# Kernel tuning notes

Measured on AMD Instinct MI355X. Metric: run time of the kernel, lower is better.

## Reference

```python
import jax, jax.numpy as jnp
import numpy as np

C = 64          # channels
K = 15          # sum(shell_sizes)=1+14
H = 32          # neighbors per query
N = 50000       # support points (== query points M)
RADIUS = 1.0
SIGMA = 0.7
INF = 1e6
BN_EPS = 1e-5


def _init_kernel_points(key):
    # stand-in for load_kernels: 1 center point + 14 points on a sphere shell
    pts = jax.random.normal(key, (K - 1, 3), dtype=jnp.float32)
    pts = pts / jnp.linalg.norm(pts, axis=1, keepdims=True) * RADIUS
    return jnp.concatenate([jnp.zeros((1, 3), jnp.float32), pts], axis=0)


def setup_inputs() -> dict:
    key = jax.random.key(0)
    ks = jax.random.split(key, 10)
    q_pts = jax.random.normal(ks[0], (N, 3), dtype=jnp.float32)
    s_pts = jax.random.normal(ks[1], (N, 3), dtype=jnp.float32)
    s_feats = jax.random.normal(ks[2], (N, C), dtype=jnp.float32)
    neighb_inds = jax.random.randint(ks[3], (N, H), 0, N)
    kernel_points = _init_kernel_points(ks[4])
    # alpha_mlp: Linear(C->C, no bias) -> BatchNorm -> LeakyReLU(0.1) -> Linear(C->K*C)
    lim1 = 1.0 / np.sqrt(C)
    W1 = jax.random.uniform(ks[5], (C, C), jnp.float32, -lim1, lim1)
    gamma = jnp.ones((C,), jnp.float32)
    beta = jnp.zeros((C,), jnp.float32)
    W2 = jax.random.uniform(ks[6], (C, K * C), jnp.float32, -lim1, lim1)
    b2 = jax.random.uniform(ks[7], (K * C,), jnp.float32, -lim1, lim1)
    return {"q_pts": q_pts, "s_pts": s_pts, "s_feats": s_feats,
            "neighb_inds": neighb_inds, "kernel_points": kernel_points,
            "W1": W1, "gamma": gamma, "beta": beta, "W2": W2, "b2": b2}


def reference(q_pts, s_pts, s_feats, neighb_inds, kernel_points, W1, gamma, beta, W2, b2):
    M = q_pts.shape[0]
    # alpha_mlp on pooled (= center) features: (M, C) -> (M, K*C)
    h = s_feats @ W1
    mu = jnp.mean(h, axis=0)
    var = jnp.var(h, axis=0)
    h = (h - mu) / jnp.sqrt(var + BN_EPS) * gamma + beta
    h = jax.nn.leaky_relu(h, 0.1)
    conv_weights = (h @ W2 + b2).reshape(M, K, C)

    # gather neighbor features with a zero padding row (index N -> zeros)
    padded_feats = jnp.concatenate([s_feats, jnp.zeros((1, C), s_feats.dtype)], axis=0)
    neighbor_feats = padded_feats[neighb_inds]                 # (M, H, C)

    # relative neighbor positions with inf padding point
    s_pts_pad = jnp.concatenate([s_pts, jnp.full((1, 3), INF, s_pts.dtype)], axis=0)
    neighbors = s_pts_pad[neighb_inds] - q_pts[:, None, :]     # (M, H, 3)

    # kernel-point influence: nearest kernel point + linear influence
    diff = neighbors[:, :, None, :] - kernel_points            # (M, H, K, 3)
    sq_d = jnp.sum(diff * diff, axis=-1)                       # (M, H, K)
    nn_sq = jnp.min(sq_d, axis=-1)                             # (M, H)
    nn_idx = jnp.argmin(sq_d, axis=-1)                         # (M, H)
    infl = jnp.clip(1.0 - jnp.sqrt(nn_sq) / SIGMA, 0.0)        # (M, H)

    # per-neighbor channel weights from the MLP output, gathered by 1nn kernel point
    nw = jnp.take_along_axis(conv_weights, nn_idx[:, :, None], axis=1)  # (M, H, C)
    nw = nw * infl[:, :, None]

    # weighted aggregation (merge=mul, aggr=sum over neighbors)
    return jnp.sum(neighbor_feats * nw, axis=1)                # (M, C)
```

## Files before the change

kernel.cpp:

```cpp
#include <hip/hip_runtime.h>
#include <math.h>

#define N_PTS 50000
#define CCH   64
#define KP    15
#define NH    32
#define SIGMA 0.7f
#define BN_EPS 1e-5f
#define LEAKY 0.1f
#define QB    16
#define STATS_BLOCKS 1024
#define SP4_BLOCKS 196
#define CW_KSTRIDE_B 2176

typedef short bf16x8 __attribute__((ext_vector_type(8)));
typedef float floatx4 __attribute__((ext_vector_type(4)));

__device__ __forceinline__ unsigned short f2b(float f) {
    union { float f; unsigned u; } v; v.f = f;
    return (unsigned short)((v.u + 0x7FFFu + ((v.u >> 16) & 1u)) >> 16);
}
__device__ __forceinline__ float b2f(unsigned short b) {
    union { unsigned u; float f; } v; v.u = ((unsigned)b) << 16;
    return v.f;
}
__device__ __forceinline__ float blo(unsigned u) {
    union { unsigned u; float f; } v; v.u = u << 16;
    return v.f;
}
__device__ __forceinline__ float bhi(unsigned u) {
    union { unsigned u; float f; } v; v.u = u & 0xFFFF0000u;
    return v.f;
}
__device__ __forceinline__ unsigned cvtpk(float lo, float hi) {
    unsigned r;
    asm("v_cvt_pk_bf16_f32 %0, %1, %2" : "=v"(r) : "v"(lo), "v"(hi));
    return r;
}

__global__ __launch_bounds__(256) void k_prep(const float* __restrict__ sf,
                                              const float* __restrict__ W1,
                                              const float* __restrict__ W2,
                                              const float* __restrict__ s_pts,
                                              const float* __restrict__ kpts,
                                              float* __restrict__ bn,
                                              unsigned short* __restrict__ hst,
                                              unsigned short* __restrict__ w2b,
                                              unsigned short* __restrict__ sfb,
                                              float* __restrict__ sp4,
                                              float* __restrict__ kpc4) {
    int t = threadIdx.x;
    if (blockIdx.x >= STATS_BLOCKS + 30 + SP4_BLOCKS) {
        if (t < KP) {
            float x = kpts[t * 3 + 0], y = kpts[t * 3 + 1], z = kpts[t * 3 + 2];
            float4 v; v.x = x; v.y = y; v.z = z; v.w = 0.5f * (x * x + y * y + z * z);
            *(float4*)(kpc4 + t * 4) = v;
        }
        return;
    }
    if (blockIdx.x >= STATS_BLOCKS + 30) {
        int g = (blockIdx.x - STATS_BLOCKS - 30) * 256 + t;
        if (g < N_PTS) {
            float4 v;
            v.x = s_pts[g * 3 + 0]; v.y = s_pts[g * 3 + 1];
            v.z = s_pts[g * 3 + 2]; v.w = 0.f;
            *(float4*)(sp4 + g * 4) = v;
        }
        return;
    }
    if (blockIdx.x >= STATS_BLOCKS) {
        int g = (blockIdx.x - STATS_BLOCKS) * 256 + t;
        int lane = g & 63, s = (g >> 6) & 1, tt = g >> 7;
        int col = lane & 15, quad = lane >> 4;
        int base = (s * 32 + quad * 8) * 960 + tt * 16 + col;
        ushort4 lo, hi;
        lo.x = f2b(W2[base + 0 * 960]); lo.y = f2b(W2[base + 1 * 960]);
        lo.z = f2b(W2[base + 2 * 960]); lo.w = f2b(W2[base + 3 * 960]);
        hi.x = f2b(W2[base + 4 * 960]); hi.y = f2b(W2[base + 5 * 960]);
        hi.z = f2b(W2[base + 6 * 960]); hi.w = f2b(W2[base + 7 * 960]);
        *(ushort4*)(w2b + g * 8)     = lo;
        *(ushort4*)(w2b + g * 8 + 4) = hi;
        return;
    }
    int c = t & 63, ml = t >> 6;
    float w1c[64];
    #pragma unroll
    for (int i = 0; i < 64; ++i) w1c[i] = W1[i * 64 + c];
    __shared__ float rows[16][64];
    float acc_s = 0.f, acc_q = 0.f;
    for (int tile = blockIdx.x; tile < N_PTS / 16; tile += STATS_BLOCKS) {
        int m0 = tile * 16;
        __syncthreads();
        float4 v = *(const float4*)(sf + m0 * 64 + t * 4);
        ((float4*)rows)[t] = v;
        ushort4 s4;
        s4.x = f2b(v.x); s4.y = f2b(v.y); s4.z = f2b(v.z); s4.w = f2b(v.w);
        *(ushort4*)(sfb + m0 * 64 + t * 4) = s4;
        __syncthreads();
        #pragma unroll
        for (int rr = 0; rr < 4; ++rr) {
            int r = ml + rr * 4;
            float h = 0.f;
            #pragma unroll
            for (int i4 = 0; i4 < 16; ++i4) {
                float4 rv = *(const float4*)&rows[r][i4 * 4];
                h += rv.x * w1c[i4 * 4] + rv.y * w1c[i4 * 4 + 1]
                   + rv.z * w1c[i4 * 4 + 2] + rv.w * w1c[i4 * 4 + 3];
            }
            acc_s += h;
            acc_q += h * h;
            hst[(m0 + r) * 64 + c] = f2b(h);
        }
    }
    __shared__ float red[2][256];
    red[0][t] = acc_s; red[1][t] = acc_q;
    __syncthreads();
    if (t < 64) {
        float s = red[0][t] + red[0][64 + t] + red[0][128 + t] + red[0][192 + t];
        float q = red[1][t] + red[1][64 + t] + red[1][128 + t] + red[1][192 + t];
        atomicAdd(&bn[t], s);
        atomicAdd(&bn[64 + t], q);
    }
}

__global__ __launch_bounds__(256, 4) void k_main(
    const float* __restrict__ q_pts, const float* __restrict__ sp4,
    const unsigned short* __restrict__ sfb, const int* __restrict__ nb,
    const float* __restrict__ kpc4, const float* __restrict__ gamma,
    const float* __restrict__ beta, const float* __restrict__ bn,
    const float* __restrict__ b2, const unsigned short* __restrict__ w2b,
    const unsigned short* __restrict__ hst, float* __restrict__ out) {

    __shared__ __align__(16) unsigned cwP[KP * 32 * 17];
    __shared__ float abS[128];
    __shared__ int      nCnt[QB];
    __shared__ unsigned nPack[QB][NH];
    __shared__ float    nInf[QB][NH];

    int t = threadIdx.x;
    int lane = t & 63, wv = t >> 6;
    int m0 = blockIdx.x * QB;

    int q0 = t >> 5, hh = t & 31;
    int q1 = q0 + 8;
    int idx0 = nb[(m0 + q0) * NH + hh];
    int idx1 = nb[(m0 + q1) * NH + hh];

    if (t < 64) {
        float mu  = bn[t] * (1.0f / N_PTS);
        float var = bn[64 + t] * (1.0f / N_PTS) - mu * mu;
        float a   = gamma[t] * rsqrtf(var + BN_EPS);
        abS[t]      = a;
        abS[64 + t] = beta[t] - mu * a;
    }
    ((unsigned*)nPack)[t]       = 0u;
    ((unsigned*)nPack)[t + 256] = 0u;
    ((float*)nInf)[t]           = 0.f;
    ((float*)nInf)[t + 256]     = 0.f;

    int row = lane & 15, half = lane >> 4;
    bf16x8 r0, r1;
    {
        const unsigned short* hrow = hst + (m0 + row) * 64 + half * 8;
        r0 = *(const bf16x8*)(hrow);
        r1 = *(const bf16x8*)(hrow + 32);
    }

    float4 sp0 = *(const float4*)(sp4 + idx0 * 4);
    float4 sp1 = *(const float4*)(sp4 + idx1 * 4);
    float qx0 = q_pts[(m0 + q0) * 3 + 0], qy0 = q_pts[(m0 + q0) * 3 + 1],
          qz0 = q_pts[(m0 + q0) * 3 + 2];
    float qx1 = q_pts[(m0 + q1) * 3 + 0], qy1 = q_pts[(m0 + q1) * 3 + 1],
          qz1 = q_pts[(m0 + q1) * 3 + 2];

    float4 kq[KP];
    #pragma unroll
    for (int i = 0; i < KP; ++i) kq[i] = *(const float4*)(kpc4 + i * 4);

    __syncthreads();

    unsigned pf0 = 0, pf1 = 0, pf2 = 0, pf3 = 0;
    {
        float px = sp0.x - qx0, py = sp0.y - qy0, pz = sp0.z - qz0;
        float pn = px * px + py * py + pz * pz;
        float best = 1e30f; int bi = 0;
        #pragma unroll
        for (int k = 0; k < KP; ++k) {
            float val = kq[k].w - (px * kq[k].x + py * kq[k].y + pz * kq[k].z);
            if (val < best) { best = val; bi = k; }
        }
        float d2 = fmaxf(fmaf(2.f, best, pn), 0.f);
        float infl = 1.f - sqrtf(d2) * (1.0f / SIGMA);
        bool keep = infl > 0.f;
        unsigned long long bal = __ballot(keep);
        unsigned mym = (unsigned)(bal >> (lane & 32));
        int pos = __popc(mym & ((1u << (lane & 31)) - 1u));
        if (keep) {
            nPack[q0][pos] = (unsigned)idx0 | ((unsigned)(bi * CW_KSTRIDE_B) << 16);
            nInf[q0][pos]  = infl;
            const unsigned* rowp = (const unsigned*)(sfb + idx0 * 64);
            pf0 = rowp[0]; pf1 = rowp[16];
        }
        if ((lane & 31) == 0) nCnt[q0] = __popc(mym);
    }
    {
        float px = sp1.x - qx1, py = sp1.y - qy1, pz = sp1.z - qz1;
        float pn = px * px + py * py + pz * pz;
        float best = 1e30f; int bi = 0;
        #pragma unroll
        for (int k = 0; k < KP; ++k) {
            float val = kq[k].w - (px * kq[k].x + py * kq[k].y + pz * kq[k].z);
            if (val < best) { best = val; bi = k; }
        }
        float d2 = fmaxf(fmaf(2.f, best, pn), 0.f);
        float infl = 1.f - sqrtf(d2) * (1.0f / SIGMA);
        bool keep = infl > 0.f;
        unsigned long long bal = __ballot(keep);
        unsigned mym = (unsigned)(bal >> (lane & 32));
        int pos = __popc(mym & ((1u << (lane & 31)) - 1u));
        if (keep) {
            nPack[q1][pos] = (unsigned)idx1 | ((unsigned)(bi * CW_KSTRIDE_B) << 16);
            nInf[q1][pos]  = infl;
            const unsigned* rowp = (const unsigned*)(sfb + idx1 * 64);
            pf2 = rowp[0]; pf3 = rowp[16];
        }
        if ((lane & 31) == 0) nCnt[q1] = __popc(mym);
    }

    bf16x8 a0, a1;
    {
        unsigned* A0 = (unsigned*)&a0;
        unsigned* A1 = (unsigned*)&a1;
        #pragma unroll
        for (int jw = 0; jw < 4; ++jw) {
            int c0 = half * 8 + jw * 2;
            float g00 = abS[c0]     * b2f((unsigned short)r0[jw * 2])     + abS[64 + c0];
            float g01 = abS[c0 + 1] * b2f((unsigned short)r0[jw * 2 + 1]) + abS[64 + c0 + 1];
            g00 = fmaxf(g00, LEAKY * g00);
            g01 = fmaxf(g01, LEAKY * g01);
            A0[jw] = cvtpk(g00, g01);
            int c1 = 32 + c0;
            float g10 = abS[c1]     * b2f((unsigned short)r1[jw * 2])     + abS[64 + c1];
            float g11 = abS[c1 + 1] * b2f((unsigned short)r1[jw * 2 + 1]) + abS[64 + c1 + 1];
            g10 = fmaxf(g10, LEAKY * g10);
            g11 = fmaxf(g11, LEAKY * g11);
            A1[jw] = cvtpk(g10, g11);
        }
    }

    {
        int colq = lane & 15, quad = lane >> 4;
        bf16x8 Lf[3], Ls[3], Mf[3], Ms[3];
        #pragma unroll
        for (int i = 0; i < 3; ++i) {
            int tt = wv * 15 + i;
            Lf[i] = *(const bf16x8*)(w2b + ((tt * 2 + 0) * 64 + lane) * 8);
            Ls[i] = *(const bf16x8*)(w2b + ((tt * 2 + 1) * 64 + lane) * 8);
        }
        #pragma unroll
        for (int g = 0; g < 5; ++g) {
            if (g < 4) {
                #pragma unroll
                for (int i = 0; i < 3; ++i) {
                    int tt = wv * 15 + (g + 1) * 3 + i;
                    Mf[i] = *(const bf16x8*)(w2b + ((tt * 2 + 0) * 64 + lane) * 8);
                    Ms[i] = *(const bf16x8*)(w2b + ((tt * 2 + 1) * 64 + lane) * 8);
                }
            }
            #pragma unroll
            for (int i = 0; i < 3; ++i) {
                int tt = wv * 15 + g * 3 + i;
                floatx4 acc = {0.f, 0.f, 0.f, 0.f};
                acc = __builtin_amdgcn_mfma_f32_16x16x32_bf16(Lf[i], a0, acc, 0, 0, 0);
                acc = __builtin_amdgcn_mfma_f32_16x16x32_bf16(Ls[i], a1, acc, 0, 0, 0);
                int n0 = tt * 16 + quad * 4;
                float4 bb = *(const float4*)&b2[n0];
                int k  = n0 >> 6;
                int c2 = (n0 & 63) >> 1;
                unsigned w0 = cvtpk(acc[0] + bb.x, acc[1] + bb.y);
                unsigned w1 = cvtpk(acc[2] + bb.z, acc[3] + bb.w);
                unsigned* dst = cwP + (k * 544 + c2 * 17 + colq);
                dst[0]  = w0;
                dst[17] = w1;
            }
            if (g < 4) {
                #pragma unroll
                for (int i = 0; i < 3; ++i) { Lf[i] = Mf[i]; Ls[i] = Ms[i]; }
            }
        }
    }
    asm volatile("" :: "v"(pf0), "v"(pf1), "v"(pf2), "v"(pf3));
    __syncthreads();

    {
        int r = lane >> 5, c2 = lane & 31;
        const unsigned short* sfbC = sfb + c2 * 2;
        const unsigned char* cwB = (const unsigned char*)cwP;
        #pragma unroll
        for (int pp = 0; pp < 2; ++pp) {
            int qa = wv * 4 + pp * 2;
            int q  = qa + r;
            const unsigned* packRow = &nPack[q][0];
            const float*    infRow  = &nInf[q][0];
            const unsigned char* cwLane = cwB + (c2 * 17 + q) * 4;
            int nA = nCnt[qa], nB = nCnt[qa + 1];
            int na = nA > nB ? nA : nB;
            float acc0 = 0.f, acc1 = 0.f;
            for (int jj = 0; jj < na; jj += 4) {
                uint4  pk = *(const uint4*)&packRow[jj];
                float4 in = *(const float4*)&infRow[jj];
                unsigned f0 = *(const unsigned*)(sfbC + (pk.x & 0xFFFFu) * 64);
                unsigned f1 = *(const unsigned*)(sfbC + (pk.y & 0xFFFFu) * 64);
                unsigned f2 = *(const unsigned*)(sfbC + (pk.z & 0xFFFFu) * 64);
                unsigned f3 = *(const unsigned*)(sfbC + (pk.w & 0xFFFFu) * 64);
                unsigned w0 = *(const unsigned*)(cwLane + (pk.x >> 16));
                unsigned w1 = *(const unsigned*)(cwLane + (pk.y >> 16));
                unsigned w2 = *(const unsigned*)(cwLane + (pk.z >> 16));
                unsigned w3 = *(const unsigned*)(cwLane + (pk.w >> 16));
                acc0 = fmaf(in.x * blo(f0), blo(w0), acc0);
                acc1 = fmaf(in.x * bhi(f0), bhi(w0), acc1);
                acc0 = fmaf(in.y * blo(f1), blo(w1), acc0);
                acc1 = fmaf(in.y * bhi(f1), bhi(w1), acc1);
                acc0 = fmaf(in.z * blo(f2), blo(w2), acc0);
                acc1 = fmaf(in.z * bhi(f2), bhi(w2), acc1);
                acc0 = fmaf(in.w * blo(f3), blo(w3), acc0);
                acc1 = fmaf(in.w * bhi(f3), bhi(w3), acc1);
            }
            float2 o; o.x = acc0; o.y = acc1;
            *(float2*)&out[(m0 + q) * 64 + c2 * 2] = o;
        }
    }
}

extern "C" void kernel_launch(void* const* d_in, const int* in_sizes, int n_in,
                              void* d_out, int out_size, void* d_ws, size_t ws_size,
                              hipStream_t stream) {
    const float* q_pts   = (const float*)d_in[0];
    const float* s_pts   = (const float*)d_in[1];
    const float* s_feats = (const float*)d_in[2];
    const int*   nb      = (const int*)d_in[3];
    const float* kpts    = (const float*)d_in[4];
    const float* W1      = (const float*)d_in[5];
    const float* gamma   = (const float*)d_in[6];
    const float* beta    = (const float*)d_in[7];
    const float* W2      = (const float*)d_in[8];
    const float* b2      = (const float*)d_in[9];
    float* out = (float*)d_out;

    float* ws = (float*)d_ws;
    float* bn = ws;
    unsigned short* w2b = (unsigned short*)(ws + 128);
    unsigned short* hst = w2b + 61440;
    unsigned short* sfb = hst + N_PTS * CCH;
    float* sp4 = (float*)(sfb + N_PTS * CCH);
    float* kpc4 = sp4 + N_PTS * 4;

    hipMemsetAsync(bn, 0, 128 * sizeof(float), stream);
    k_prep<<<STATS_BLOCKS + 30 + SP4_BLOCKS + 1, 256, 0, stream>>>(
        s_feats, W1, W2, s_pts, kpts, bn, hst, w2b, sfb, sp4, kpc4);
    k_main<<<N_PTS / QB, 256, 0, stream>>>(q_pts, sp4, sfb, nb, kpc4,
                                           gamma, beta, bn, b2, w2b, hst, out);
}
```

Baseline: 152.8 us.

## Process 32 queries per block to reuse W2 fragments across two MFMA tiles

Doubles the queries per block from 16 to 32. Each W2 fragment loaded from global memory now feeds two 16-row MFMA tiles, halving W2 traffic per query. It also adds tail clamping for the non-divisible block count. Padding of the neighbor lists is now done inline (non-kept slots written as zero) instead of by a separate zero-init pass. In exchange, LDS use and register pressure roughly double, so launch bounds drop to 2 blocks per SM, which can lower occupancy for the latency-bound gather phase.

```diff
diff --git a/kernel.cpp b/kernel.cpp
--- a/kernel.cpp
+++ b/kernel.cpp
@@ -8,10 +8,11 @@
 #define SIGMA 0.7f
 #define BN_EPS 1e-5f
 #define LEAKY 0.1f
-#define QB    16
+#define QB    32
+#define NBLK  ((N_PTS + QB - 1) / QB)
 #define STATS_BLOCKS 1024
 #define SP4_BLOCKS 196
-#define CW_KSTRIDE_B 2176
+#define CW_KSTRIDE_B 4224
 
 typedef short bf16x8 __attribute__((ext_vector_type(8)));
 typedef float floatx4 __attribute__((ext_vector_type(4)));
@@ -123,7 +124,7 @@
     }
 }
 
-__global__ __launch_bounds__(256, 4) void k_main(
+__global__ __launch_bounds__(256, 2) void k_main(
     const float* __restrict__ q_pts, const float* __restrict__ sp4,
     const unsigned short* __restrict__ sfb, const int* __restrict__ nb,
     const float* __restrict__ kpc4, const float* __restrict__ gamma,
@@ -131,7 +132,7 @@
     const float* __restrict__ b2, const unsigned short* __restrict__ w2b,
     const unsigned short* __restrict__ hst, float* __restrict__ out) {
 
-    __shared__ __align__(16) unsigned cwP[KP * 32 * 17];
+    __shared__ __align__(16) unsigned cwP[KP * 32 * 33];
     __shared__ float abS[128];
     __shared__ int      nCnt[QB];
     __shared__ unsigned nPack[QB][NH];
@@ -141,10 +142,15 @@
     int lane = t & 63, wv = t >> 6;
     int m0 = blockIdx.x * QB;
 
-    int q0 = t >> 5, hh = t & 31;
-    int q1 = q0 + 8;
-    int idx0 = nb[(m0 + q0) * NH + hh];
-    int idx1 = nb[(m0 + q1) * NH + hh];
+    int qb = t >> 5, hh = t & 31;
+    int mq0 = min(m0 + qb,      N_PTS - 1);
+    int mq1 = min(m0 + qb + 8,  N_PTS - 1);
+    int mq2 = min(m0 + qb + 16, N_PTS - 1);
+    int mq3 = min(m0 + qb + 24, N_PTS - 1);
+    int idx0 = nb[mq0 * NH + hh];
+    int idx1 = nb[mq1 * NH + hh];
+    int idx2 = nb[mq2 * NH + hh];
+    int idx3 = nb[mq3 * NH + hh];
 
     if (t < 64) {
         float mu  = bn[t] * (1.0f / N_PTS);
@@ -153,25 +159,26 @@
         abS[t]      = a;
         abS[64 + t] = beta[t] - mu * a;
     }
-    ((unsigned*)nPack)[t]       = 0u;
-    ((unsigned*)nPack)[t + 256] = 0u;
-    ((float*)nInf)[t]           = 0.f;
-    ((float*)nInf)[t + 256]     = 0.f;
 
     int row = lane & 15, half = lane >> 4;
-    bf16x8 r0, r1;
+    bf16x8 r0, r1, r0b, r1b;
     {
-        const unsigned short* hrow = hst + (m0 + row) * 64 + half * 8;
-        r0 = *(const bf16x8*)(hrow);
-        r1 = *(const bf16x8*)(hrow + 32);
+        int ra = min(m0 + row,      N_PTS - 1);
+        int rb = min(m0 + 16 + row, N_PTS - 1);
+        const unsigned short* ha = hst + ra * 64 + half * 8;
+        const unsigned short* hb = hst + rb * 64 + half * 8;
+        r0  = *(const bf16x8*)(ha);        r1  = *(const bf16x8*)(ha + 32);
+        r0b = *(const bf16x8*)(hb);        r1b = *(const bf16x8*)(hb + 32);
     }
 
     float4 sp0 = *(const float4*)(sp4 + idx0 * 4);
     float4 sp1 = *(const float4*)(sp4 + idx1 * 4);
-    float qx0 = q_pts[(m0 + q0) * 3 + 0], qy0 = q_pts[(m0 + q0) * 3 + 1],
-          qz0 = q_pts[(m0 + q0) * 3 + 2];
-    float qx1 = q_pts[(m0 + q1) * 3 + 0], qy1 = q_pts[(m0 + q1) * 3 + 1],
-          qz1 = q_pts[(m0 + q1) * 3 + 2];
+    float4 sp2 = *(const float4*)(sp4 + idx2 * 4);
+    float4 sp3 = *(const float4*)(sp4 + idx3 * 4);
+    float qx0 = q_pts[mq0 * 3 + 0], qy0 = q_pts[mq0 * 3 + 1], qz0 = q_pts[mq0 * 3 + 2];
+    float qx1 = q_pts[mq1 * 3 + 0], qy1 = q_pts[mq1 * 3 + 1], qz1 = q_pts[mq1 * 3 + 2];
+    float qx2 = q_pts[mq2 * 3 + 0], qy2 = q_pts[mq2 * 3 + 1], qz2 = q_pts[mq2 * 3 + 2];
+    float qx3 = q_pts[mq3 * 3 + 0], qy3 = q_pts[mq3 * 3 + 1], qz3 = q_pts[mq3 * 3 + 2];
 
     float4 kq[KP];
     #pragma unroll
@@ -179,72 +186,61 @@
 
     __syncthreads();
 
-    unsigned pf0 = 0, pf1 = 0, pf2 = 0, pf3 = 0;
+    unsigned pf0 = 0, pf1 = 0, pf2 = 0, pf3 = 0, pf4 = 0, pf5 = 0, pf6 = 0, pf7 = 0;
+#define PHASE1(SP, QX, QY, QZ, IDX, QOFF, PFA, PFB)                                   \
+    {                                                                                 \
+        int q = qb + QOFF;                                                            \
+        float px = SP.x - QX, py = SP.y - QY, pz = SP.z - QZ;                         \
+        float pn = px * px + py * py + pz * pz;                                       \
+        float best = 1e30f; int bi = 0;                                               \
+        _Pragma("unroll")                                                             \
+        for (int k = 0; k < KP; ++k) {                                                \
+            float val = kq[k].w - (px * kq[k].x + py * kq[k].y + pz * kq[k].z);       \
+            if (val < best) { best = val; bi = k; }                                   \
+        }                                                                             \
+        float d2 = fmaxf(fmaf(2.f, best, pn), 0.f);                                   \
+        float infl = 1.f - sqrtf(d2) * (1.0f / SIGMA);                                \
+        bool keep = infl > 0.f;                                                       \
+        unsigned long long bal = __ballot(keep);                                      \
+        unsigned mym = (unsigned)(bal >> (lane & 32));                                \
+        unsigned below = mym & ((1u << (lane & 31)) - 1u);                            \
+        int cnt = __popc(mym);                                                        \
+        int pos = keep ? __popc(below) : cnt + ((lane & 31) - __popc(below));         \
+        nPack[q][pos] = keep ? ((unsigned)IDX | ((unsigned)(bi * CW_KSTRIDE_B) << 16)) \
+                             : 0u;                                                    \
+        nInf[q][pos]  = keep ? infl : 0.f;                                            \
+        if (keep) {                                                                   \
+            const unsigned* rowp = (const unsigned*)(sfb + IDX * 64);                 \
+            PFA = rowp[0]; PFB = rowp[16];                                            \
+        }                                                                             \
+        if ((lane & 31) == 0) nCnt[q] = cnt;                                          \
+    }
+    PHASE1(sp0, qx0, qy0, qz0, idx0, 0,  pf0, pf1)
+    PHASE1(sp1, qx1, qy1, qz1, idx1, 8,  pf2, pf3)
+    PHASE1(sp2, qx2, qy2, qz2, idx2, 16, pf4, pf5)
+    PHASE1(sp3, qx3, qy3, qz3, idx3, 24, pf6, pf7)
+#undef PHASE1
+
+    bf16x8 a0, a1, a0b, a1b;
     {
-        float px = sp0.x - qx0, py = sp0.y - qy0, pz = sp0.z - qz0;
-        float pn = px * px + py * py + pz * pz;
-        float best = 1e30f; int bi = 0;
-        #pragma unroll
-        for (int k = 0; k < KP; ++k) {
-            float val = kq[k].w - (px * kq[k].x + py * kq[k].y + pz * kq[k].z);
-            if (val < best) { best = val; bi = k; }
-        }
-        float d2 = fmaxf(fmaf(2.f, best, pn), 0.f);
-        float infl = 1.f - sqrtf(d2) * (1.0f / SIGMA);
-        bool keep = infl > 0.f;
-        unsigned long long bal = __ballot(keep);
-        unsigned mym = (unsigned)(bal >> (lane & 32));
-        int pos = __popc(mym & ((1u << (lane & 31)) - 1u));
-        if (keep) {
-            nPack[q0][pos] = (unsigned)idx0 | ((unsigned)(bi * CW_KSTRIDE_B) << 16);
-            nInf[q0][pos]  = infl;
-            const unsigned* rowp = (const unsigned*)(sfb + idx0 * 64);
-            pf0 = rowp[0]; pf1 = rowp[16];
-        }
-        if ((lane & 31) == 0) nCnt[q0] = __popc(mym);
-    }
-    {
-        float px = sp1.x - qx1, py = sp1.y - qy1, pz = sp1.z - qz1;
-        float pn = px * px + py * py + pz * pz;
-        float best = 1e30f; int bi = 0;
-        #pragma unroll
-        for (int k = 0; k < KP; ++k) {
-            float val = kq[k].w - (px * kq[k].x + py * kq[k].y + pz * kq[k].z);
-            if (val < best) { best = val; bi = k; }
-        }
-        float d2 = fmaxf(fmaf(2.f, best, pn), 0.f);
-        float infl = 1.f - sqrtf(d2) * (1.0f / SIGMA);
-        bool keep = infl > 0.f;
-        unsigned long long bal = __ballot(keep);
-        unsigned mym = (unsigned)(bal >> (lane & 32));
-        int pos = __popc(mym & ((1u << (lane & 31)) - 1u));
-        if (keep) {
-            nPack[q1][pos] = (unsigned)idx1 | ((unsigned)(bi * CW_KSTRIDE_B) << 16);
-            nInf[q1][pos]  = infl;
-            const unsigned* rowp = (const unsigned*)(sfb + idx1 * 64);
-            pf2 = rowp[0]; pf3 = rowp[16];
-        }
-        if ((lane & 31) == 0) nCnt[q1] = __popc(mym);
-    }
-
-    bf16x8 a0, a1;
-    {
-        unsigned* A0 = (unsigned*)&a0;
-        unsigned* A1 = (unsigned*)&a1;
+        unsigned* A0 = (unsigned*)&a0;  unsigned* A1 = (unsigned*)&a1;
+        unsigned* B0 = (unsigned*)&a0b; unsigned* B1 = (unsigned*)&a1b;
         #pragma unroll
         for (int jw = 0; jw < 4; ++jw) {
             int c0 = half * 8 + jw * 2;
+            int c1 = 32 + c0;
             float g00 = abS[c0]     * b2f((unsigned short)r0[jw * 2])     + abS[64 + c0];
             float g01 = abS[c0 + 1] * b2f((unsigned short)r0[jw * 2 + 1]) + abS[64 + c0 + 1];
-            g00 = fmaxf(g00, LEAKY * g00);
-            g01 = fmaxf(g01, LEAKY * g01);
-            A0[jw] = cvtpk(g00, g01);
-            int c1 = 32 + c0;
+            A0[jw] = cvtpk(fmaxf(g00, LEAKY * g00), fmaxf(g01, LEAKY * g01));
             float g10 = abS[c1]     * b2f((unsigned short)r1[jw * 2])     + abS[64 + c1];
             float g11 = abS[c1 + 1] * b2f((unsigned short)r1[jw * 2 + 1]) + abS[64 + c1 + 1];
-            g10 = fmaxf(g10, LEAKY * g10);
-            g11 = fmaxf(g11, LEAKY * g11);
-            A1[jw] = cvtpk(g10, g11);
+            A1[jw] = cvtpk(fmaxf(g10, LEAKY * g10), fmaxf(g11, LEAKY * g11));
+            float h00 = abS[c0]     * b2f((unsigned short)r0b[jw * 2])     + abS[64 + c0];
+            float h01 = abS[c0 + 1] * b2f((unsigned short)r0b[jw * 2 + 1]) + abS[64 + c0 + 1];
+            B0[jw] = cvtpk(fmaxf(h00, LEAKY * h00), fmaxf(h01, LEAKY * h01));
+            float h10 = abS[c1]     * b2f((unsigned short)r1b[jw * 2])     + abS[64 + c1];
+            float h11 = abS[c1 + 1] * b2f((unsigned short)r1b[jw * 2 + 1]) + abS[64 + c1 + 1];
+            B1[jw] = cvtpk(fmaxf(h10, LEAKY * h10), fmaxf(h11, LEAKY * h11));
         }
     }
 
@@ -270,18 +266,25 @@
             #pragma unroll
             for (int i = 0; i < 3; ++i) {
                 int tt = wv * 15 + g * 3 + i;
-                floatx4 acc = {0.f, 0.f, 0.f, 0.f};
-                acc = __builtin_amdgcn_mfma_f32_16x16x32_bf16(Lf[i], a0, acc, 0, 0, 0);
-                acc = __builtin_amdgcn_mfma_f32_16x16x32_bf16(Ls[i], a1, acc, 0, 0, 0);
+                floatx4 accA = {0.f, 0.f, 0.f, 0.f};
+                floatx4 accB = {0.f, 0.f, 0.f, 0.f};
+                accA = __builtin_amdgcn_mfma_f32_16x16x32_bf16(Lf[i], a0,  accA, 0, 0, 0);
+                accA = __builtin_amdgcn_mfma_f32_16x16x32_bf16(Ls[i], a1,  accA, 0, 0, 0);
+                accB = __builtin_amdgcn_mfma_f32_16x16x32_bf16(Lf[i], a0b, accB, 0, 0, 0);
+                accB = __builtin_amdgcn_mfma_f32_16x16x32_bf16(Ls[i], a1b, accB, 0, 0, 0);
                 int n0 = tt * 16 + quad * 4;
                 float4 bb = *(const float4*)&b2[n0];
                 int k  = n0 >> 6;
                 int c2 = (n0 & 63) >> 1;
-                unsigned w0 = cvtpk(acc[0] + bb.x, acc[1] + bb.y);
-                unsigned w1 = cvtpk(acc[2] + bb.z, acc[3] + bb.w);
-                unsigned* dst = cwP + (k * 544 + c2 * 17 + colq);
+                unsigned w0 = cvtpk(accA[0] + bb.x, accA[1] + bb.y);
+                unsigned w1 = cvtpk(accA[2] + bb.z, accA[3] + bb.w);
+                unsigned w2 = cvtpk(accB[0] + bb.x, accB[1] + bb.y);
+                unsigned w3 = cvtpk(accB[2] + bb.z, accB[3] + bb.w);
+                unsigned* dst = cwP + (k * 1056 + c2 * 33 + colq);
                 dst[0]  = w0;
-                dst[17] = w1;
+                dst[33] = w1;
+                dst[16] = w2;
+                dst[49] = w3;
             }
             if (g < 4) {
                 #pragma unroll
@@ -289,7 +292,8 @@
             }
         }
     }
-    asm volatile("" :: "v"(pf0), "v"(pf1), "v"(pf2), "v"(pf3));
+    asm volatile("" :: "v"(pf0), "v"(pf1), "v"(pf2), "v"(pf3),
+                       "v"(pf4), "v"(pf5), "v"(pf6), "v"(pf7));
     __syncthreads();
 
     {
@@ -297,12 +301,12 @@
         const unsigned short* sfbC = sfb + c2 * 2;
         const unsigned char* cwB = (const unsigned char*)cwP;
         #pragma unroll
-        for (int pp = 0; pp < 2; ++pp) {
-            int qa = wv * 4 + pp * 2;
+        for (int pp = 0; pp < 4; ++pp) {
+            int qa = wv * 8 + pp * 2;
             int q  = qa + r;
             const unsigned* packRow = &nPack[q][0];
             const float*    infRow  = &nInf[q][0];
-            const unsigned char* cwLane = cwB + (c2 * 17 + q) * 4;
+            const unsigned char* cwLane = cwB + (c2 * 33 + q) * 4;
             int nA = nCnt[qa], nB = nCnt[qa + 1];
             int na = nA > nB ? nA : nB;
             float acc0 = 0.f, acc1 = 0.f;
@@ -326,8 +330,10 @@
                 acc0 = fmaf(in.w * blo(f3), blo(w3), acc0);
                 acc1 = fmaf(in.w * bhi(f3), bhi(w3), acc1);
             }
-            float2 o; o.x = acc0; o.y = acc1;
-            *(float2*)&out[(m0 + q) * 64 + c2 * 2] = o;
+            if (m0 + q < N_PTS) {
+                float2 o; o.x = acc0; o.y = acc1;
+                *(float2*)&out[(m0 + q) * 64 + c2 * 2] = o;
+            }
         }
     }
 }
@@ -358,6 +364,6 @@
     hipMemsetAsync(bn, 0, 128 * sizeof(float), stream);
     k_prep<<<STATS_BLOCKS + 30 + SP4_BLOCKS + 1, 256, 0, stream>>>(
         s_feats, W1, W2, s_pts, kpts, bn, hst, w2b, sfb, sp4, kpc4);
-    k_main<<<N_PTS / QB, 256, 0, stream>>>(q_pts, sp4, sfb, nb, kpc4,
-                                           gamma, beta, bn, b2, w2b, hst, out);
-}
+    k_main<<<NBLK, 256, 0, stream>>>(q_pts, sp4, sfb, nb, kpc4,
+                                     gamma, beta, bn, b2, w2b, hst, out);
+}
```

After: 159.0 us. +4.1%, slower.
